# Optimization experiments

Hardware: AMD Instinct MI355X
Metric: run time of the kernel (lower is better)

The kernel has to match this reference:

```python
import jax, jax.numpy as jnp
import numpy as np

B, T_HIST, D, H, STEPS = 2048, 15, 64, 128, 20
MAX_STEPS = 48           # max adaptive steps per unit time interval
DT0, RTOL, ATOL = 0.1, 1e-3, 1e-6
SAFETY, FMIN, FMAX = 0.9, 0.2, 10.0

# Tsit5 (Tsitouras 2011) tableau
A21 = 0.161
A31, A32 = -0.008480655492356989, 0.335480655492357
A41, A42, A43 = 2.8971530571054935, -6.359448489975075, 4.3622954328695815
A51, A52, A53, A54 = 5.325864828439257, -11.748883564062828, 7.4955393428898365, -0.09249506636175525
A61, A62, A63, A64, A65 = 5.86145544294642, -12.92096931784711, 8.159367898576159, -0.071584973281401, -0.028269050394068383
B1, B2, B3, B4, B5, B6 = 0.09646076681806523, 0.01, 0.4798896504144996, 1.379008574103742, -3.290069515436081, 2.324710524099774
E1, E2, E3, E4, E5, E6, E7 = (-0.00178001105222577714, -0.0008164344596567469, 0.007880878010261995,
                              -0.1447110071732629, 0.5823571654525552, -0.45808210592918697, 0.015151515151515152)


def _mlp(y, W1, b1, W2, b2, W3, b3):
    h = jax.nn.softplus(y @ W1.T + b1)
    h = jax.nn.softplus(h @ W2.T + b2)
    return h @ W3.T + b3


def _solve(y0, W1, b1, W2, b2, W3, b3, steps):
    f = lambda y: _mlp(y, W1, b1, W2, b2, W3, b3)  # batched vector field [B,D]->[B,D]
    Bn = y0.shape[0]

    def segment(carry, t1):
        y, dt = carry
        t = jnp.full((Bn,), t1 - 1.0, y0.dtype)
        done = jnp.zeros((Bn,), bool)

        def body(state, _):
            t, y, dt, done = state
            dt_c = jnp.minimum(dt, t1 - t)          # clip to segment end
            h = dt_c[:, None]
            k1 = f(y)
            k2 = f(y + h * (A21 * k1))
            k3 = f(y + h * (A31 * k1 + A32 * k2))
            k4 = f(y + h * (A41 * k1 + A42 * k2 + A43 * k3))
            k5 = f(y + h * (A51 * k1 + A52 * k2 + A53 * k3 + A54 * k4))
            k6 = f(y + h * (A61 * k1 + A62 * k2 + A63 * k3 + A64 * k4 + A65 * k5))
            y5 = y + h * (B1 * k1 + B2 * k2 + B3 * k3 + B4 * k4 + B5 * k5 + B6 * k6)
            k7 = f(y5)
            err = h * (E1 * k1 + E2 * k2 + E3 * k3 + E4 * k4 + E5 * k5 + E6 * k6 + E7 * k7)
            scale = ATOL + RTOL * jnp.maximum(jnp.abs(y), jnp.abs(y5))
            err_norm = jnp.sqrt(jnp.mean((err / scale) ** 2, axis=-1))  # [B]
            accept = (err_norm <= 1.0) & (~done)
            factor = jnp.clip(SAFETY * jnp.maximum(err_norm, 1e-10) ** (-0.2), FMIN, FMAX)
            t_new = jnp.where(accept, t + dt_c, t)
            y_new = jnp.where(accept[:, None], y5, y)
            dt_new = jnp.where(done, dt, dt_c * factor)
            done_new = done | (t_new >= t1 - 1e-8)
            return (t_new, y_new, dt_new, done_new), None

        (t, y, dt, done), _ = jax.lax.scan(jax.checkpoint(body), (t, y, dt, done), None, length=MAX_STEPS)
        return (y, dt), y

    ts1 = jnp.arange(1, steps + 1, dtype=y0.dtype)
    dt0 = jnp.full((Bn,), DT0, y0.dtype)
    (_, _), ys = jax.lax.scan(segment, (y0, dt0), ts1)  # ys: [steps, B, D]
    return jnp.transpose(ys, (1, 0, 2))                  # [B, steps, D]


def setup_inputs() -> dict:
    key = jax.random.key(0)
    ks = jax.random.split(key, 7)
    history = jax.random.normal(ks[0], (B, T_HIST, D), jnp.float32)
    # small-scale init keeps the vector field mild so adaptive steps converge
    W1 = jax.random.normal(ks[1], (H, D), jnp.float32) * (0.5 / np.sqrt(D))
    b1 = jax.random.normal(ks[2], (H,), jnp.float32) * 0.05
    W2 = jax.random.normal(ks[3], (H, H), jnp.float32) * (0.5 / np.sqrt(H))
    b2 = jax.random.normal(ks[4], (H,), jnp.float32) * 0.05
    W3 = jax.random.normal(ks[5], (D, H), jnp.float32) * (0.1 / np.sqrt(H))
    b3 = jax.random.normal(ks[6], (D,), jnp.float32) * 0.05
    return {"history": history, "W1": W1, "b1": b1, "W2": W2, "b2": b2, "W3": W3, "b3": b3, "steps": STEPS}


def reference(history, W1, b1, W2, b2, W3, b3, steps):
    y0 = history[:, -1]  # NeuralODE uses only the last history state
    return _solve(y0, W1, b1, W2, b2, W3, b3, steps)
```

## Files before the change

### kernel.cpp

```cpp
#include <hip/hip_runtime.h>
#include <math.h>

#define NB    2048
#define NSEG  20
#define MAXIT 48
#define CH    544
#define BLKS  136

typedef __attribute__((ext_vector_type(8))) short bf8_t;
typedef __attribute__((ext_vector_type(4))) float f32x4;

#define cA21 ((float)0.161)
#define cA31 ((float)-0.008480655492356989)
#define cA32 ((float)0.335480655492357)
#define cA41 ((float)2.8971530571054935)
#define cA42 ((float)-6.359448489975075)
#define cA43 ((float)4.3622954328695815)
#define cA51 ((float)5.325864828439257)
#define cA52 ((float)-11.748883564062828)
#define cA53 ((float)7.4955393428898365)
#define cA54 ((float)-0.09249506636175525)
#define cA61 ((float)5.86145544294642)
#define cA62 ((float)-12.92096931784711)
#define cA63 ((float)8.159367898576159)
#define cA64 ((float)-0.071584973281401)
#define cA65 ((float)-0.028269050394068383)
#define cB1  ((float)0.09646076681806523)
#define cB2  ((float)0.01)
#define cB3  ((float)0.4798896504144996)
#define cB4  ((float)1.379008574103742)
#define cB5  ((float)-3.290069515436081)
#define cB6  ((float)2.324710524099774)
#define cE1  ((float)-0.001780011052225777)
#define cE2  ((float)-0.0008164344596567469)
#define cE3  ((float)0.007880878010261995)
#define cE4  ((float)-0.1447110071732629)
#define cE5  ((float)0.5823571654525552)
#define cE6  ((float)-0.45808210592918697)
#define cE7  ((float)0.015151515151515152)

__device__ __forceinline__ void split2(float x, short &hi, short &lo) {
    unsigned u = __float_as_uint(x);
    hi = (short)(u >> 16);
    float r = x - __uint_as_float(u & 0xFFFF0000u);
    lo = (short)(__float_as_uint(r) >> 16);
}

__device__ __forceinline__ float softplus_f(float x) {
    float t = exp2f(-fabsf(x) * 1.442695040888963f);
    return fmaxf(x, 0.0f) + log2f(1.0f + t) * 0.6931471805599453f;
}

__device__ __forceinline__ unsigned pk(short a, short b) {
    return ((unsigned)(unsigned short)a) | (((unsigned)(unsigned short)b) << 16);
}

__device__ __forceinline__ float fold8(float x) {
    int r = __builtin_amdgcn_update_dpp(__float_as_int(x), __float_as_int(x),
                                        0x128, 0xF, 0xF, false);
    return x + __int_as_float(r);
}

__global__ __launch_bounds__(512)
void ode_kernel(const float* __restrict__ history,
                const float* __restrict__ W1, const float* __restrict__ b1,
                const float* __restrict__ W2, const float* __restrict__ b2,
                const float* __restrict__ W3, const float* __restrict__ b3,
                float* __restrict__ out)
{
    __shared__ alignas(16) short h1B[4 * CH];
    __shared__ alignas(16) short h2B[4 * CH];
    __shared__ float rrP[32];

    const int tid  = threadIdx.x;
    const int wave = tid >> 6, lane = tid & 63;
    const int quad = lane >> 4, col = lane & 15;
    const int jb   = 16 * wave + 4 * quad;
    const int esel = col >> 3;
    const int e    = col & 7;
    const int j0   = jb + 2 * esel;
    const size_t elemIdx = (size_t)(blockIdx.x * 8 + e);
    const int zi   = (j0 >> 5) * CH + ((j0 >> 3) & 3) * BLKS + e * 8 + (j0 & 7);
    const int boff = quad * BLKS + col * 8;

    bf8_t A2h[4], A2l[4];
#pragma unroll
    for (int c = 0; c < 4; ++c) {
        const float* p = W2 + (size_t)(16 * wave + col) * 128 + 32 * c + 8 * quad;
        bf8_t h, l;
#pragma unroll
        for (int j = 0; j < 8; ++j) { short hs, ls; split2(p[j], hs, ls); h[j] = hs; l[j] = ls; }
        A2h[c] = h; A2l[c] = l;
    }
    bf8_t A3h[4], A3l[4];
    float b3v0 = 0.f, b3v1 = 0.f;
    if (wave < 4) {
#pragma unroll
        for (int c = 0; c < 4; ++c) {
            const float* p = W3 + (size_t)(16 * wave + col) * 128 + 32 * c + 8 * quad;
            bf8_t h, l;
#pragma unroll
            for (int j = 0; j < 8; ++j) { short hs, ls; split2(p[j], hs, ls); h[j] = hs; l[j] = ls; }
            A3h[c] = h; A3l[c] = l;
        }
        b3v0 = b3[j0]; b3v1 = b3[j0 + 1];
    } else {
        bf8_t z = {0, 0, 0, 0, 0, 0, 0, 0};
#pragma unroll
        for (int c = 0; c < 4; ++c) { A3h[c] = z; A3l[c] = z; }
    }
    const f32x4 b2f = *(const f32x4*)(b2 + jb);
    const float b1v0 = b1[j0], b1v1 = b1[j0 + 1];

    bf8_t Mh[4], Ml[4];
    {
        float accM[4][8];
#pragma unroll
        for (int cc = 0; cc < 4; ++cc)
#pragma unroll
            for (int j = 0; j < 8; ++j) accM[cc][j] = 0.f;
        const float* w1r = W1 + (size_t)(16 * wave + col) * 64;
#pragma unroll 2
        for (int d = 0; d < 64; ++d) {
            float wv = w1r[d];
            const float* w3r = W3 + (size_t)d * 128 + 8 * quad;
#pragma unroll
            for (int cc = 0; cc < 4; ++cc) {
                f32x4 va = *(const f32x4*)(w3r + 32 * cc);
                f32x4 vb = *(const f32x4*)(w3r + 32 * cc + 4);
#pragma unroll
                for (int j = 0; j < 4; ++j) {
                    accM[cc][j]     = fmaf(wv, va[j], accM[cc][j]);
                    accM[cc][4 + j] = fmaf(wv, vb[j], accM[cc][4 + j]);
                }
            }
        }
#pragma unroll
        for (int cc = 0; cc < 4; ++cc) {
            bf8_t hh, ll;
#pragma unroll
            for (int j = 0; j < 8; ++j) { short hs, ls; split2(accM[cc][j], hs, ls); hh[j] = hs; ll[j] = ls; }
            Mh[cc] = hh; Ml[cc] = ll;
        }
    }

    auto gemm = [&](const bf8_t* Ah, const bf8_t* Al, const short* Bc, int nch) -> f32x4 {
        f32x4 a0 = {0.f, 0.f, 0.f, 0.f}, a1 = a0;
#pragma unroll
        for (int c = 0; c < nch; ++c) {
            bf8_t b = *(const bf8_t*)(Bc + c * CH + boff);
            a0 = __builtin_amdgcn_mfma_f32_16x16x32_bf16(Ah[c], b, a0, 0, 0, 0);
            a1 = __builtin_amdgcn_mfma_f32_16x16x32_bf16(Al[c], b, a1, 0, 0, 0);
        }
        f32x4 s;
#pragma unroll
        for (int r = 0; r < 4; ++r) s[r] = a0[r] + a1[r];
        return s;
    };

    float zy0, zy1, cc0, cc1;
    float ys0 = 0.f, ys1 = 0.f;
    {
        bf8_t W1h[2], W1l[2];
#pragma unroll
        for (int c = 0; c < 2; ++c) {
            const float* p = W1 + (size_t)(16 * wave + col) * 64 + 32 * c + 8 * quad;
            bf8_t h, l;
#pragma unroll
            for (int j = 0; j < 8; ++j) { short hs, ls; split2(p[j], hs, ls); h[j] = hs; l[j] = ls; }
            W1h[c] = h; W1l[c] = l;
        }
        if (wave < 4) {
            float2 yy = *(const float2*)(history + (elemIdx * 15 + 14) * 64 + j0);
            ys0 = yy.x; ys1 = yy.y;
            short ha, la, hb, lb;
            split2(ys0, ha, la); split2(ys1, hb, lb);
            *(unsigned*)(h1B + zi)      = pk(ha, hb);
            *(unsigned*)(h1B + zi + 64) = pk(la, lb);
            split2(b3v0, ha, la); split2(b3v1, hb, lb);
            *(unsigned*)(h2B + zi)      = pk(ha, hb);
            *(unsigned*)(h2B + zi + 64) = pk(la, lb);
        }
        __syncthreads();
        f32x4 sz = gemm(W1h, W1l, h1B, 2);
        f32x4 sc = gemm(W1h, W1l, h2B, 2);
        float f0 = fold8(sz[0]), f1 = fold8(sz[1]), f2 = fold8(sz[2]), f3 = fold8(sz[3]);
        zy0 = (esel ? f2 : f0) + b1v0;
        zy1 = (esel ? f3 : f1) + b1v1;
        float g0 = fold8(sc[0]), g1 = fold8(sc[1]), g2 = fold8(sc[2]), g3 = fold8(sc[3]);
        cc0 = esel ? g2 : g0;
        cc1 = esel ? g3 : g1;
        __syncthreads();
    }

    auto epi = [&](f32x4 s, f32x4 bias, short* Bn) {
        float t0 = fold8(s[0]) + bias[0];
        float t1 = fold8(s[1]) + bias[1];
        float t2 = fold8(s[2]) + bias[2];
        float t3 = fold8(s[3]) + bias[3];
        float x0 = esel ? t2 : t0;
        float x1 = esel ? t3 : t1;
        float p0 = softplus_f(x0), p1 = softplus_f(x1);
        short h0s, l0s, h1s, l1s;
        split2(p0, h0s, l0s);
        split2(p1, h1s, l1s);
        *(unsigned*)(Bn + zi)      = pk(h0s, h1s);
        *(unsigned*)(Bn + zi + 64) = pk(l0s, l1s);
    };

    auto do_eval = [&](float za, float zb, float &ua, float &ub, float &ka, float &kb) {
        float p0 = softplus_f(za), p1 = softplus_f(zb);
        short h0s, l0s, h1s, l1s;
        split2(p0, h0s, l0s);
        split2(p1, h1s, l1s);
        *(unsigned*)(h1B + zi)      = pk(h0s, h1s);
        *(unsigned*)(h1B + zi + 64) = pk(l0s, l1s);
        __syncthreads();
        f32x4 s2 = gemm(A2h, A2l, h1B, 4);
        epi(s2, b2f, h2B);
        __syncthreads();
        f32x4 zz = {0.f, 0.f, 0.f, 0.f};
        f32x4 m0 = zz, m1 = zz, w0 = zz, w1 = zz;
#pragma unroll
        for (int c = 0; c < 4; ++c) {
            bf8_t b = *(const bf8_t*)(h2B + c * CH + boff);
            m0 = __builtin_amdgcn_mfma_f32_16x16x32_bf16(Mh[c],  b, m0, 0, 0, 0);
            m1 = __builtin_amdgcn_mfma_f32_16x16x32_bf16(Ml[c],  b, m1, 0, 0, 0);
            w0 = __builtin_amdgcn_mfma_f32_16x16x32_bf16(A3h[c], b, w0, 0, 0, 0);
            w1 = __builtin_amdgcn_mfma_f32_16x16x32_bf16(A3l[c], b, w1, 0, 0, 0);
        }
        float f0 = fold8(m0[0] + m1[0]);
        float f1 = fold8(m0[1] + m1[1]);
        float f2 = fold8(m0[2] + m1[2]);
        float f3 = fold8(m0[3] + m1[3]);
        ua = (esel ? f2 : f0) + cc0;
        ub = (esel ? f3 : f1) + cc1;
        float g0 = fold8(w0[0] + w1[0]);
        float g1 = fold8(w0[1] + w1[1]);
        float g2 = fold8(w0[2] + w1[2]);
        float g3 = fold8(w0[3] + w1[3]);
        ka = (esel ? g2 : g0) + b3v0;
        kb = (esel ? g3 : g1) + b3v1;
    };

    float dt = 0.1f;
    float u1a, u1b, u2a, u2b, u3a, u3b, u4a, u4b, u5a, u5b, u6a, u6b;
    float k1a = 0.f, k1b = 0.f, k2a, k2b, k3a, k3b, k4a, k4b, k5a, k5b, k6a, k6b;

    do_eval(zy0, zy1, u1a, u1b, k1a, k1b);

#pragma unroll 1
    for (int seg = 1; seg <= NSEG; ++seg) {
        const float t1 = (float)seg;
        float t = t1 - 1.0f;
        bool done = false;

#pragma unroll 1
        for (int it = 0; it < MAXIT; ++it) {
            const float dt_c = fminf(dt, t1 - t);
            const float h = dt_c;
            float y50 = 0.f, y51 = 0.f, k7a = 0.f, k7b = 0.f;
            float u7a = 0.f, u7b = 0.f, zy5a = 0.f, zy5b = 0.f;

#pragma unroll 1
            for (int st = 2; st <= 7; ++st) {
                float sa, sb;
                switch (st) {
                    case 2: sa = cA21 * u1a;
                            sb = cA21 * u1b; break;
                    case 3: sa = fmaf(cA31, u1a, cA32 * u2a);
                            sb = fmaf(cA31, u1b, cA32 * u2b); break;
                    case 4: sa = fmaf(cA41, u1a, fmaf(cA42, u2a, cA43 * u3a));
                            sb = fmaf(cA41, u1b, fmaf(cA42, u2b, cA43 * u3b)); break;
                    case 5: sa = fmaf(cA51, u1a, fmaf(cA52, u2a, fmaf(cA53, u3a, cA54 * u4a)));
                            sb = fmaf(cA51, u1b, fmaf(cA52, u2b, fmaf(cA53, u3b, cA54 * u4b))); break;
                    case 6: sa = fmaf(cA61, u1a, fmaf(cA62, u2a, fmaf(cA63, u3a, fmaf(cA64, u4a, cA65 * u5a))));
                            sb = fmaf(cA61, u1b, fmaf(cA62, u2b, fmaf(cA63, u3b, fmaf(cA64, u4b, cA65 * u5b)))); break;
                    default: sa = fmaf(cB1, u1a, fmaf(cB2, u2a, fmaf(cB3, u3a, fmaf(cB4, u4a, fmaf(cB5, u5a, cB6 * u6a)))));
                             sb = fmaf(cB1, u1b, fmaf(cB2, u2b, fmaf(cB3, u3b, fmaf(cB4, u4b, fmaf(cB5, u5b, cB6 * u6b))))); break;
                }
                float za = fmaf(h, sa, zy0);
                float zb = fmaf(h, sb, zy1);
                if (st == 7) {
                    zy5a = za; zy5b = zb;
                    float ta = fmaf(cB1, k1a, fmaf(cB2, k2a, fmaf(cB3, k3a, fmaf(cB4, k4a, fmaf(cB5, k5a, cB6 * k6a)))));
                    float tb = fmaf(cB1, k1b, fmaf(cB2, k2b, fmaf(cB3, k3b, fmaf(cB4, k4b, fmaf(cB5, k5b, cB6 * k6b)))));
                    y50 = fmaf(h, ta, ys0);
                    y51 = fmaf(h, tb, ys1);
                }
                float ua, ub, ka, kb;
                do_eval(za, zb, ua, ub, ka, kb);
                switch (st) {
                    case 2: u2a = ua; u2b = ub; k2a = ka; k2b = kb; break;
                    case 3: u3a = ua; u3b = ub; k3a = ka; k3b = kb; break;
                    case 4: u4a = ua; u4b = ub; k4a = ka; k4b = kb; break;
                    case 5: u5a = ua; u5b = ub; k5a = ka; k5b = kb; break;
                    case 6: u6a = ua; u6b = ub; k6a = ka; k6b = kb; break;
                    default: u7a = ua; u7b = ub; k7a = ka; k7b = kb; break;
                }
            }

            float rr2 = 0.f;
            if (wave < 4) {
                float es0 = fmaf(cE1, k1a, fmaf(cE2, k2a, fmaf(cE3, k3a,
                            fmaf(cE4, k4a, fmaf(cE5, k5a, fmaf(cE6, k6a, cE7 * k7a))))));
                float es1 = fmaf(cE1, k1b, fmaf(cE2, k2b, fmaf(cE3, k3b,
                            fmaf(cE4, k4b, fmaf(cE5, k5b, fmaf(cE6, k6b, cE7 * k7b))))));
                float err0 = h * es0, err1 = h * es1;
                float sc0 = fmaf(1e-3f, fmaxf(fabsf(ys0), fabsf(y50)), 1e-6f);
                float sc1 = fmaf(1e-3f, fmaxf(fabsf(ys1), fabsf(y51)), 1e-6f);
                float r0 = err0 / sc0, r1 = err1 / sc1;
                rr2 = fmaf(r0, r0, r1 * r1);
            }
            rr2 += __shfl_xor(rr2, 16, 64);
            rr2 += __shfl_xor(rr2, 32, 64);
            rr2 = fold8(rr2);
            if (wave < 4 && lane < 8) rrP[wave * 8 + lane] = rr2;
            __syncthreads();
            float rs = ((rrP[e] + rrP[8 + e]) + rrP[16 + e]) + rrP[24 + e];
            float en = sqrtf(rs * (1.0f / 64.0f));

            bool accept = (en <= 1.0f) && !done;
            float fac = 0.9f * exp2f(-0.2f * log2f(fmaxf(en, 1e-10f)));
            fac = fminf(fmaxf(fac, 0.2f), 10.0f);

            if (accept) {
                t += dt_c;
                zy0 = zy5a; zy1 = zy5b;
                u1a = u7a;  u1b = u7b;
                if (wave < 4) { ys0 = y50; ys1 = y51; k1a = k7a; k1b = k7b; }
            }
            if (!done) dt = dt_c * fac;
            done = done || (t >= t1 - 1e-8f);
            if (__all(done)) break;
        }

        if (wave < 4) {
            float2 yy; yy.x = ys0; yy.y = ys1;
            *(float2*)(out + (elemIdx * NSEG + (seg - 1)) * 64 + j0) = yy;
        }
    }
}

extern "C" void kernel_launch(void* const* d_in, const int* in_sizes, int n_in,
                              void* d_out, int out_size, void* d_ws, size_t ws_size,
                              hipStream_t stream) {
    const float* history = (const float*)d_in[0];
    const float* W1 = (const float*)d_in[1];
    const float* b1 = (const float*)d_in[2];
    const float* W2 = (const float*)d_in[3];
    const float* b2 = (const float*)d_in[4];
    const float* W3 = (const float*)d_in[5];
    const float* b3 = (const float*)d_in[6];
    float* out = (float*)d_out;

    ode_kernel<<<dim3(NB / 8), dim3(512), 0, stream>>>(history, W1, b1, W2, b2, W3, b3, out);
}
```

Measured before the change: 307.4 us.

## Specialize waves: four compute y-space k, four compute all 128 hidden u

Splits the eight waves by role. Waves 0-3 compute the output-space derivative k through W3. Waves 4-7 compute the 128-wide hidden-space update u through the fused W1·W3 matrix, covering two row tiles each. Before, every wave ran both the M and the A3 MFMAs, and waves 4-7 carried zero A3 weights. Now the unused MFMAs are removed and the per-wave stage work is rebalanced, at the cost of more registers for MhB/MlB in the u waves and a divergent branch around the second-layer phase.

```diff
diff --git a/kernel.cpp b/kernel.cpp
--- a/kernel.cpp
+++ b/kernel.cpp
@@ -75,12 +75,20 @@
     const int tid  = threadIdx.x;
     const int wave = tid >> 6, lane = tid & 63;
     const int quad = lane >> 4, col = lane & 15;
-    const int jb   = 16 * wave + 4 * quad;
+    const int w4   = wave & 3;
+    const bool isU = wave >= 4;
     const int esel = col >> 3;
     const int e    = col & 7;
+    const int jb   = 16 * wave + 4 * quad;
     const int j0   = jb + 2 * esel;
+    const int j0A  = 16 * w4 + 4 * quad + 2 * esel;
+    const int j0B  = 64 + j0A;
     const size_t elemIdx = (size_t)(blockIdx.x * 8 + e);
-    const int zi   = (j0 >> 5) * CH + ((j0 >> 3) & 3) * BLKS + e * 8 + (j0 & 7);
+
+    auto bidx = [&](int j) { return (j >> 5) * CH + ((j >> 3) & 3) * BLKS + e * 8 + (j & 7); };
+    const int zi   = bidx(j0);
+    const int ziA  = bidx(j0A);
+    const int ziB  = bidx(j0B);
     const int boff = quad * BLKS + col * 8;
 
     bf8_t A2h[4], A2l[4];
@@ -92,9 +100,19 @@
         for (int j = 0; j < 8; ++j) { short hs, ls; split2(p[j], hs, ls); h[j] = hs; l[j] = ls; }
         A2h[c] = h; A2l[c] = l;
     }
+    const f32x4 b2f = *(const f32x4*)(b2 + jb);
+
     bf8_t A3h[4], A3l[4];
-    float b3v0 = 0.f, b3v1 = 0.f;
-    if (wave < 4) {
+    bf8_t MhA[4], MlA[4], MhB[4], MlB[4];
+    float b3v0 = 0.f, b3v1 = 0.f, ys0 = 0.f, ys1 = 0.f;
+    f32x4 zy  = {0.f, 0.f, 0.f, 0.f};
+    f32x4 ccv = {0.f, 0.f, 0.f, 0.f};
+    {
+        bf8_t z = {0, 0, 0, 0, 0, 0, 0, 0};
+#pragma unroll
+        for (int c = 0; c < 4; ++c) { A3h[c] = z; A3l[c] = z; MhA[c] = z; MlA[c] = z; MhB[c] = z; MlB[c] = z; }
+    }
+    if (!isU) {
 #pragma unroll
         for (int c = 0; c < 4; ++c) {
             const float* p = W3 + (size_t)(16 * wave + col) * 128 + 32 * c + 8 * quad;
@@ -103,44 +121,39 @@
             for (int j = 0; j < 8; ++j) { short hs, ls; split2(p[j], hs, ls); h[j] = hs; l[j] = ls; }
             A3h[c] = h; A3l[c] = l;
         }
-        b3v0 = b3[j0]; b3v1 = b3[j0 + 1];
+        b3v0 = b3[j0A]; b3v1 = b3[j0A + 1];
     } else {
-        bf8_t z = {0, 0, 0, 0, 0, 0, 0, 0};
-#pragma unroll
-        for (int c = 0; c < 4; ++c) { A3h[c] = z; A3l[c] = z; }
-    }
-    const f32x4 b2f = *(const f32x4*)(b2 + jb);
-    const float b1v0 = b1[j0], b1v1 = b1[j0 + 1];
-
-    bf8_t Mh[4], Ml[4];
-    {
-        float accM[4][8];
-#pragma unroll
-        for (int cc = 0; cc < 4; ++cc)
-#pragma unroll
-            for (int j = 0; j < 8; ++j) accM[cc][j] = 0.f;
-        const float* w1r = W1 + (size_t)(16 * wave + col) * 64;
+#pragma unroll 1
+        for (int tt = 0; tt < 2; ++tt) {
+            float accM[4][8];
+#pragma unroll
+            for (int cc = 0; cc < 4; ++cc)
+#pragma unroll
+                for (int j = 0; j < 8; ++j) accM[cc][j] = 0.f;
+            const float* w1r = W1 + (size_t)(64 * tt + 16 * w4 + col) * 64;
 #pragma unroll 2
-        for (int d = 0; d < 64; ++d) {
-            float wv = w1r[d];
-            const float* w3r = W3 + (size_t)d * 128 + 8 * quad;
+            for (int d = 0; d < 64; ++d) {
+                float wv = w1r[d];
+                const float* w3r = W3 + (size_t)d * 128 + 8 * quad;
+#pragma unroll
+                for (int cc = 0; cc < 4; ++cc) {
+                    f32x4 va = *(const f32x4*)(w3r + 32 * cc);
+                    f32x4 vb = *(const f32x4*)(w3r + 32 * cc + 4);
+#pragma unroll
+                    for (int j = 0; j < 4; ++j) {
+                        accM[cc][j]     = fmaf(wv, va[j], accM[cc][j]);
+                        accM[cc][4 + j] = fmaf(wv, vb[j], accM[cc][4 + j]);
+                    }
+                }
+            }
 #pragma unroll
             for (int cc = 0; cc < 4; ++cc) {
-                f32x4 va = *(const f32x4*)(w3r + 32 * cc);
-                f32x4 vb = *(const f32x4*)(w3r + 32 * cc + 4);
-#pragma unroll
-                for (int j = 0; j < 4; ++j) {
-                    accM[cc][j]     = fmaf(wv, va[j], accM[cc][j]);
-                    accM[cc][4 + j] = fmaf(wv, vb[j], accM[cc][4 + j]);
-                }
-            }
-        }
-#pragma unroll
-        for (int cc = 0; cc < 4; ++cc) {
-            bf8_t hh, ll;
-#pragma unroll
-            for (int j = 0; j < 8; ++j) { short hs, ls; split2(accM[cc][j], hs, ls); hh[j] = hs; ll[j] = ls; }
-            Mh[cc] = hh; Ml[cc] = ll;
+                bf8_t hh, ll;
+#pragma unroll
+                for (int j = 0; j < 8; ++j) { short hs, ls; split2(accM[cc][j], hs, ls); hh[j] = hs; ll[j] = ls; }
+                if (tt == 0) { MhA[cc] = hh; MlA[cc] = ll; }
+                else         { MhB[cc] = hh; MlB[cc] = ll; }
+            }
         }
     }
 
@@ -157,41 +170,6 @@
         for (int r = 0; r < 4; ++r) s[r] = a0[r] + a1[r];
         return s;
     };
-
-    float zy0, zy1, cc0, cc1;
-    float ys0 = 0.f, ys1 = 0.f;
-    {
-        bf8_t W1h[2], W1l[2];
-#pragma unroll
-        for (int c = 0; c < 2; ++c) {
-            const float* p = W1 + (size_t)(16 * wave + col) * 64 + 32 * c + 8 * quad;
-            bf8_t h, l;
-#pragma unroll
-            for (int j = 0; j < 8; ++j) { short hs, ls; split2(p[j], hs, ls); h[j] = hs; l[j] = ls; }
-            W1h[c] = h; W1l[c] = l;
-        }
-        if (wave < 4) {
-            float2 yy = *(const float2*)(history + (elemIdx * 15 + 14) * 64 + j0);
-            ys0 = yy.x; ys1 = yy.y;
-            short ha, la, hb, lb;
-            split2(ys0, ha, la); split2(ys1, hb, lb);
-            *(unsigned*)(h1B + zi)      = pk(ha, hb);
-            *(unsigned*)(h1B + zi + 64) = pk(la, lb);
-            split2(b3v0, ha, la); split2(b3v1, hb, lb);
-            *(unsigned*)(h2B + zi)      = pk(ha, hb);
-            *(unsigned*)(h2B + zi + 64) = pk(la, lb);
-        }
-        __syncthreads();
-        f32x4 sz = gemm(W1h, W1l, h1B, 2);
-        f32x4 sc = gemm(W1h, W1l, h2B, 2);
-        float f0 = fold8(sz[0]), f1 = fold8(sz[1]), f2 = fold8(sz[2]), f3 = fold8(sz[3]);
-        zy0 = (esel ? f2 : f0) + b1v0;
-        zy1 = (esel ? f3 : f1) + b1v1;
-        float g0 = fold8(sc[0]), g1 = fold8(sc[1]), g2 = fold8(sc[2]), g3 = fold8(sc[3]);
-        cc0 = esel ? g2 : g0;
-        cc1 = esel ? g3 : g1;
-        __syncthreads();
-    }
 
     auto epi = [&](f32x4 s, f32x4 bias, short* Bn) {
         float t0 = fold8(s[0]) + bias[0];
@@ -208,100 +186,197 @@
         *(unsigned*)(Bn + zi + 64) = pk(l0s, l1s);
     };
 
-    auto do_eval = [&](float za, float zb, float &ua, float &ub, float &ka, float &kb) {
-        float p0 = softplus_f(za), p1 = softplus_f(zb);
-        short h0s, l0s, h1s, l1s;
-        split2(p0, h0s, l0s);
-        split2(p1, h1s, l1s);
-        *(unsigned*)(h1B + zi)      = pk(h0s, h1s);
-        *(unsigned*)(h1B + zi + 64) = pk(l0s, l1s);
-        __syncthreads();
+    auto spw = [&](f32x4 zs) {
+        float p0 = softplus_f(zs[0]), p1 = softplus_f(zs[1]);
+        float p2 = softplus_f(zs[2]), p3 = softplus_f(zs[3]);
+        short ha, la, hb, lb;
+        split2(p0, ha, la); split2(p1, hb, lb);
+        *(unsigned*)(h1B + ziA)      = pk(ha, hb);
+        *(unsigned*)(h1B + ziA + 64) = pk(la, lb);
+        split2(p2, ha, la); split2(p3, hb, lb);
+        *(unsigned*)(h1B + ziB)      = pk(ha, hb);
+        *(unsigned*)(h1B + ziB + 64) = pk(la, lb);
+    };
+
+    auto phB = [&](f32x4 &uo, float &ka, float &kb) {
+        if (!isU) {
+            f32x4 z = {0.f, 0.f, 0.f, 0.f};
+            f32x4 w0 = z, w1 = z;
+#pragma unroll
+            for (int c = 0; c < 4; ++c) {
+                bf8_t b = *(const bf8_t*)(h2B + c * CH + boff);
+                w0 = __builtin_amdgcn_mfma_f32_16x16x32_bf16(A3h[c], b, w0, 0, 0, 0);
+                w1 = __builtin_amdgcn_mfma_f32_16x16x32_bf16(A3l[c], b, w1, 0, 0, 0);
+            }
+            float g0 = fold8(w0[0] + w1[0]);
+            float g1 = fold8(w0[1] + w1[1]);
+            float g2 = fold8(w0[2] + w1[2]);
+            float g3 = fold8(w0[3] + w1[3]);
+            ka = (esel ? g2 : g0) + b3v0;
+            kb = (esel ? g3 : g1) + b3v1;
+        } else {
+            f32x4 z = {0.f, 0.f, 0.f, 0.f};
+            f32x4 aA0 = z, aA1 = z, aB0 = z, aB1 = z;
+#pragma unroll
+            for (int c = 0; c < 4; ++c) {
+                bf8_t b = *(const bf8_t*)(h2B + c * CH + boff);
+                aA0 = __builtin_amdgcn_mfma_f32_16x16x32_bf16(MhA[c], b, aA0, 0, 0, 0);
+                aA1 = __builtin_amdgcn_mfma_f32_16x16x32_bf16(MlA[c], b, aA1, 0, 0, 0);
+                aB0 = __builtin_amdgcn_mfma_f32_16x16x32_bf16(MhB[c], b, aB0, 0, 0, 0);
+                aB1 = __builtin_amdgcn_mfma_f32_16x16x32_bf16(MlB[c], b, aB1, 0, 0, 0);
+            }
+            float fA0 = fold8(aA0[0] + aA1[0]);
+            float fA1 = fold8(aA0[1] + aA1[1]);
+            float fA2 = fold8(aA0[2] + aA1[2]);
+            float fA3 = fold8(aA0[3] + aA1[3]);
+            float fB0 = fold8(aB0[0] + aB1[0]);
+            float fB1 = fold8(aB0[1] + aB1[1]);
+            float fB2 = fold8(aB0[2] + aB1[2]);
+            float fB3 = fold8(aB0[3] + aB1[3]);
+            uo[0] = (esel ? fA2 : fA0) + ccv[0];
+            uo[1] = (esel ? fA3 : fA1) + ccv[1];
+            uo[2] = (esel ? fB2 : fB0) + ccv[2];
+            uo[3] = (esel ? fB3 : fB1) + ccv[3];
+        }
+    };
+
+    if (!isU) {
+        float2 yy = *(const float2*)(history + (elemIdx * 15 + 14) * 64 + j0A);
+        ys0 = yy.x; ys1 = yy.y;
+        short ha, la, hb, lb;
+        split2(ys0, ha, la); split2(ys1, hb, lb);
+        *(unsigned*)(h1B + ziA)      = pk(ha, hb);
+        *(unsigned*)(h1B + ziA + 64) = pk(la, lb);
+        split2(b3v0, ha, la); split2(b3v1, hb, lb);
+        *(unsigned*)(h2B + ziA)      = pk(ha, hb);
+        *(unsigned*)(h2B + ziA + 64) = pk(la, lb);
+    }
+    __syncthreads();
+    if (isU) {
+        bf8_t W1h[2], W1l[2];
+#pragma unroll 1
+        for (int tt = 0; tt < 2; ++tt) {
+            const int jt = tt ? j0B : j0A;
+#pragma unroll
+            for (int c = 0; c < 2; ++c) {
+                const float* p = W1 + (size_t)(64 * tt + 16 * w4 + col) * 64 + 32 * c + 8 * quad;
+                bf8_t h, l;
+#pragma unroll
+                for (int j = 0; j < 8; ++j) { short hs, ls; split2(p[j], hs, ls); h[j] = hs; l[j] = ls; }
+                W1h[c] = h; W1l[c] = l;
+            }
+            f32x4 sz = gemm(W1h, W1l, h1B, 2);
+            f32x4 sc = gemm(W1h, W1l, h2B, 2);
+            float f0 = fold8(sz[0]), f1 = fold8(sz[1]), f2 = fold8(sz[2]), f3 = fold8(sz[3]);
+            float g0 = fold8(sc[0]), g1 = fold8(sc[1]), g2 = fold8(sc[2]), g3 = fold8(sc[3]);
+            if (tt == 0) {
+                zy[0] = (esel ? f2 : f0) + b1[jt];
+                zy[1] = (esel ? f3 : f1) + b1[jt + 1];
+                ccv[0] = esel ? g2 : g0;
+                ccv[1] = esel ? g3 : g1;
+            } else {
+                zy[2] = (esel ? f2 : f0) + b1[jt];
+                zy[3] = (esel ? f3 : f1) + b1[jt + 1];
+                ccv[2] = esel ? g2 : g0;
+                ccv[3] = esel ? g3 : g1;
+            }
+        }
+    }
+    __syncthreads();
+    if (isU) spw(zy);
+    __syncthreads();
+
+    float dt = 0.1f;
+    f32x4 u1 = {0.f, 0.f, 0.f, 0.f}, u2 = u1, u3 = u1, u4 = u1, u5 = u1, u6 = u1, u7 = u1;
+    float k1a = 0.f, k1b = 0.f, k2a = 0.f, k2b = 0.f, k3a = 0.f, k3b = 0.f;
+    float k4a = 0.f, k4b = 0.f, k5a = 0.f, k5b = 0.f, k6a = 0.f, k6b = 0.f;
+    float k7a = 0.f, k7b = 0.f;
+
+    {
         f32x4 s2 = gemm(A2h, A2l, h1B, 4);
         epi(s2, b2f, h2B);
         __syncthreads();
-        f32x4 zz = {0.f, 0.f, 0.f, 0.f};
-        f32x4 m0 = zz, m1 = zz, w0 = zz, w1 = zz;
-#pragma unroll
-        for (int c = 0; c < 4; ++c) {
-            bf8_t b = *(const bf8_t*)(h2B + c * CH + boff);
-            m0 = __builtin_amdgcn_mfma_f32_16x16x32_bf16(Mh[c],  b, m0, 0, 0, 0);
-            m1 = __builtin_amdgcn_mfma_f32_16x16x32_bf16(Ml[c],  b, m1, 0, 0, 0);
-            w0 = __builtin_amdgcn_mfma_f32_16x16x32_bf16(A3h[c], b, w0, 0, 0, 0);
-            w1 = __builtin_amdgcn_mfma_f32_16x16x32_bf16(A3l[c], b, w1, 0, 0, 0);
-        }
-        float f0 = fold8(m0[0] + m1[0]);
-        float f1 = fold8(m0[1] + m1[1]);
-        float f2 = fold8(m0[2] + m1[2]);
-        float f3 = fold8(m0[3] + m1[3]);
-        ua = (esel ? f2 : f0) + cc0;
-        ub = (esel ? f3 : f1) + cc1;
-        float g0 = fold8(w0[0] + w1[0]);
-        float g1 = fold8(w0[1] + w1[1]);
-        float g2 = fold8(w0[2] + w1[2]);
-        float g3 = fold8(w0[3] + w1[3]);
-        ka = (esel ? g2 : g0) + b3v0;
-        kb = (esel ? g3 : g1) + b3v1;
-    };
-
-    float dt = 0.1f;
-    float u1a, u1b, u2a, u2b, u3a, u3b, u4a, u4b, u5a, u5b, u6a, u6b;
-    float k1a = 0.f, k1b = 0.f, k2a, k2b, k3a, k3b, k4a, k4b, k5a, k5b, k6a, k6b;
-
-    do_eval(zy0, zy1, u1a, u1b, k1a, k1b);
+        phB(u1, k1a, k1b);
+    }
 
 #pragma unroll 1
     for (int seg = 1; seg <= NSEG; ++seg) {
-        const float t1 = (float)seg;
-        float t = t1 - 1.0f;
+        const float tEnd = (float)seg;
+        float t = tEnd - 1.0f;
         bool done = false;
 
 #pragma unroll 1
         for (int it = 0; it < MAXIT; ++it) {
-            const float dt_c = fminf(dt, t1 - t);
+            const float dt_c = fminf(dt, tEnd - t);
             const float h = dt_c;
-            float y50 = 0.f, y51 = 0.f, k7a = 0.f, k7b = 0.f;
-            float u7a = 0.f, u7b = 0.f, zy5a = 0.f, zy5b = 0.f;
+            f32x4 zy5 = {0.f, 0.f, 0.f, 0.f};
+            float y50 = 0.f, y51 = 0.f;
+
+            if (isU) {
+                f32x4 zn;
+#pragma unroll
+                for (int r = 0; r < 4; ++r) zn[r] = fmaf(h, cA21 * u1[r], zy[r]);
+                spw(zn);
+            }
+            __syncthreads();
 
 #pragma unroll 1
             for (int st = 2; st <= 7; ++st) {
-                float sa, sb;
-                switch (st) {
-                    case 2: sa = cA21 * u1a;
-                            sb = cA21 * u1b; break;
-                    case 3: sa = fmaf(cA31, u1a, cA32 * u2a);
-                            sb = fmaf(cA31, u1b, cA32 * u2b); break;
-                    case 4: sa = fmaf(cA41, u1a, fmaf(cA42, u2a, cA43 * u3a));
-                            sb = fmaf(cA41, u1b, fmaf(cA42, u2b, cA43 * u3b)); break;
-                    case 5: sa = fmaf(cA51, u1a, fmaf(cA52, u2a, fmaf(cA53, u3a, cA54 * u4a)));
-                            sb = fmaf(cA51, u1b, fmaf(cA52, u2b, fmaf(cA53, u3b, cA54 * u4b))); break;
-                    case 6: sa = fmaf(cA61, u1a, fmaf(cA62, u2a, fmaf(cA63, u3a, fmaf(cA64, u4a, cA65 * u5a))));
-                            sb = fmaf(cA61, u1b, fmaf(cA62, u2b, fmaf(cA63, u3b, fmaf(cA64, u4b, cA65 * u5b)))); break;
-                    default: sa = fmaf(cB1, u1a, fmaf(cB2, u2a, fmaf(cB3, u3a, fmaf(cB4, u4a, fmaf(cB5, u5a, cB6 * u6a)))));
-                             sb = fmaf(cB1, u1b, fmaf(cB2, u2b, fmaf(cB3, u3b, fmaf(cB4, u4b, fmaf(cB5, u5b, cB6 * u6b))))); break;
+                {
+                    f32x4 s2 = gemm(A2h, A2l, h1B, 4);
+                    epi(s2, b2f, h2B);
                 }
-                float za = fmaf(h, sa, zy0);
-                float zb = fmaf(h, sb, zy1);
-                if (st == 7) {
-                    zy5a = za; zy5b = zb;
-                    float ta = fmaf(cB1, k1a, fmaf(cB2, k2a, fmaf(cB3, k3a, fmaf(cB4, k4a, fmaf(cB5, k5a, cB6 * k6a)))));
-                    float tb = fmaf(cB1, k1b, fmaf(cB2, k2b, fmaf(cB3, k3b, fmaf(cB4, k4b, fmaf(cB5, k5b, cB6 * k6b)))));
-                    y50 = fmaf(h, ta, ys0);
-                    y51 = fmaf(h, tb, ys1);
+                __syncthreads();
+                f32x4 uo = {0.f, 0.f, 0.f, 0.f};
+                float ka = 0.f, kb = 0.f;
+                phB(uo, ka, kb);
+                if (isU) {
+                    switch (st) {
+                        case 2: u2 = uo; break;
+                        case 3: u3 = uo; break;
+                        case 4: u4 = uo; break;
+                        case 5: u5 = uo; break;
+                        case 6: u6 = uo; break;
+                        default: u7 = uo; break;
+                    }
+                } else {
+                    switch (st) {
+                        case 2: k2a = ka; k2b = kb; break;
+                        case 3: k3a = ka; k3b = kb; break;
+                        case 4: k4a = ka; k4b = kb; break;
+                        case 5: k5a = ka; k5b = kb; break;
+                        case 6: k6a = ka; k6b = kb; break;
+                        default: k7a = ka; k7b = kb; break;
+                    }
                 }
-                float ua, ub, ka, kb;
-                do_eval(za, zb, ua, ub, ka, kb);
-                switch (st) {
-                    case 2: u2a = ua; u2b = ub; k2a = ka; k2b = kb; break;
-                    case 3: u3a = ua; u3b = ub; k3a = ka; k3b = kb; break;
-                    case 4: u4a = ua; u4b = ub; k4a = ka; k4b = kb; break;
-                    case 5: u5a = ua; u5b = ub; k5a = ka; k5b = kb; break;
-                    case 6: u6a = ua; u6b = ub; k6a = ka; k6b = kb; break;
-                    default: u7a = ua; u7b = ub; k7a = ka; k7b = kb; break;
+                if (st < 7) {
+                    if (isU) {
+                        f32x4 zn;
+#pragma unroll
+                        for (int r = 0; r < 4; ++r) {
+                            float sv;
+                            switch (st) {
+                                case 2: sv = fmaf(cA31, u1[r], cA32 * u2[r]); break;
+                                case 3: sv = fmaf(cA41, u1[r], fmaf(cA42, u2[r], cA43 * u3[r])); break;
+                                case 4: sv = fmaf(cA51, u1[r], fmaf(cA52, u2[r], fmaf(cA53, u3[r], cA54 * u4[r]))); break;
+                                case 5: sv = fmaf(cA61, u1[r], fmaf(cA62, u2[r], fmaf(cA63, u3[r], fmaf(cA64, u4[r], cA65 * u5[r])))); break;
+                                default: sv = fmaf(cB1, u1[r], fmaf(cB2, u2[r], fmaf(cB3, u3[r], fmaf(cB4, u4[r], fmaf(cB5, u5[r], cB6 * u6[r]))))); break;
+                            }
+                            zn[r] = fmaf(h, sv, zy[r]);
+                        }
+                        if (st == 6) zy5 = zn;
+                        spw(zn);
+                    }
+                    __syncthreads();
                 }
             }
 
             float rr2 = 0.f;
-            if (wave < 4) {
+            if (!isU) {
+                float ta = fmaf(cB1, k1a, fmaf(cB2, k2a, fmaf(cB3, k3a, fmaf(cB4, k4a, fmaf(cB5, k5a, cB6 * k6a)))));
+                float tb = fmaf(cB1, k1b, fmaf(cB2, k2b, fmaf(cB3, k3b, fmaf(cB4, k4b, fmaf(cB5, k5b, cB6 * k6b)))));
+                y50 = fmaf(h, ta, ys0);
+                y51 = fmaf(h, tb, ys1);
                 float es0 = fmaf(cE1, k1a, fmaf(cE2, k2a, fmaf(cE3, k3a,
                             fmaf(cE4, k4a, fmaf(cE5, k5a, fmaf(cE6, k6a, cE7 * k7a))))));
                 float es1 = fmaf(cE1, k1b, fmaf(cE2, k2b, fmaf(cE3, k3b,
@@ -315,7 +390,7 @@
             rr2 += __shfl_xor(rr2, 16, 64);
             rr2 += __shfl_xor(rr2, 32, 64);
             rr2 = fold8(rr2);
-            if (wave < 4 && lane < 8) rrP[wave * 8 + lane] = rr2;
+            if (!isU && lane < 8) rrP[wave * 8 + lane] = rr2;
             __syncthreads();
             float rs = ((rrP[e] + rrP[8 + e]) + rrP[16 + e]) + rrP[24 + e];
             float en = sqrtf(rs * (1.0f / 64.0f));
@@ -326,18 +401,17 @@
 
             if (accept) {
                 t += dt_c;
-                zy0 = zy5a; zy1 = zy5b;
-                u1a = u7a;  u1b = u7b;
-                if (wave < 4) { ys0 = y50; ys1 = y51; k1a = k7a; k1b = k7b; }
+                if (!isU) { ys0 = y50; ys1 = y51; k1a = k7a; k1b = k7b; }
+                else      { zy = zy5; u1 = u7; }
             }
             if (!done) dt = dt_c * fac;
-            done = done || (t >= t1 - 1e-8f);
+            done = done || (t >= tEnd - 1e-8f);
             if (__all(done)) break;
         }
 
-        if (wave < 4) {
+        if (!isU) {
             float2 yy; yy.x = ys0; yy.y = ys1;
-            *(float2*)(out + (elemIdx * NSEG + (seg - 1)) * 64 + j0) = yy;
+            *(float2*)(out + (elemIdx * NSEG + (seg - 1)) * 64 + j0A) = yy;
         }
     }
 }
```

New measurement: 362.8 us. 1.18x slower.
